# Performance work log

Measured on AMD Instinct MI355X. Metric: run time of the kernel, lower is better.

Reference implementation:

```python
import jax, jax.numpy as jnp
import numpy as np
import math


def setup_inputs() -> dict:
    B, L, D, P, V = 4, 4096, 512, 128, 8
    key = jax.random.key(0)
    ki = iter(jax.random.split(key, 40))
    def rn(shape, s=0.02):
        return jax.random.normal(next(ki), shape, jnp.float32) * s
    z = lambda *s: jnp.zeros(s, jnp.float32)
    return dict(
        x=jax.random.normal(next(ki), (B, L, D), jnp.float32),
        W_omega=rn((D, D)), b_omega=z(D),
        omega_scale=jnp.full((D,), 0.01, jnp.float32),
        W_pi1=rn((D, D)), b_pi1=z(D), W_pi2=rn((D, D)), b_pi2=z(D),
        W_m1v=rn((D, D)), b_m1v=z(D),
        W_m1o=rn((D, D)), b_m1o=z(D),
        W_mag=rn((D, D)), b_mag=z(D),
        mag_scale=jnp.asarray(5.0, jnp.float32),
        W_qoff=rn((D, D)), b_qoff=z(D),
        W_kenc=rn((D, P)), b_kenc=z(P),
        W_venc=rn((D, V)), b_venc=z(V),
        W_sk1=rn((2 * D, D)), b_sk1=z(D),
        W_sk2=rn((D, P)), b_sk2=z(P),
        W_sg=rn((D, 1)), b_sg=z(1),
        W_kvo=rn((V, D)), b_kvo=z(D),
        ln_g=jnp.ones((4 * D,), jnp.float32), ln_b=z(4 * D),
        W_o1=rn((4 * D, 2 * D)), b_o1=z(2 * D),
        W_o2=rn((2 * D, D)), b_o2=z(D),
    )


def _lin(h, W, b):
    return h @ W + b


def _gelu(h):
    return jax.nn.gelu(h, approximate=False)  # torch nn.GELU default (erf)


def _forward(x, W_omega, b_omega, omega_scale, W_pi1, b_pi1, W_pi2, b_pi2,
             W_m1v, b_m1v, W_m1o, b_m1o, W_mag, b_mag, mag_scale,
             W_qoff, b_qoff, W_kenc, b_kenc, W_venc, b_venc,
             W_sk1, b_sk1, W_sk2, b_sk2, W_sg, b_sg, W_kvo, b_kvo,
             ln_g, ln_b, W_o1, b_o1, W_o2, b_o2):
    B, L, D = x.shape
    P = W_kenc.shape[1]
    # --- evolving phases ---
    omega_scaled = _lin(x, W_omega, b_omega) * jnp.abs(omega_scale)
    phi_init = _lin(_gelu(_lin(x, W_pi1, b_pi1)), W_pi2, b_pi2)
    phi = phi_init + jnp.cumsum(omega_scaled, axis=1)
    cos_phi, sin_phi = jnp.cos(phi), jnp.sin(phi)
    # --- memory 1: positional phasor memory ---
    v1 = _lin(x, W_m1v, b_m1v)
    magnitude = jax.nn.sigmoid(_lin(x, W_mag, b_mag)) * jnp.abs(mag_scale)
    wv1 = magnitude * v1
    sqrt_mag = jnp.sqrt(jnp.cumsum(magnitude, axis=1) + 1e-8)
    mem1_cos = jnp.cumsum(wv1 * cos_phi, axis=1) / sqrt_mag
    mem1_sin = jnp.cumsum(wv1 * sin_phi, axis=1) / sqrt_mag
    phi_q = phi + _lin(x, W_qoff, b_qoff)
    pos_ret = (mem1_cos * jnp.cos(phi_q) + mem1_sin * jnp.sin(phi_q)) / math.sqrt(D)
    pos_out = _lin(pos_ret, W_m1o, b_m1o)
    # --- memory 2: key/value phasor binding ---
    query_phase = jnp.tanh(_lin(x, W_kenc, b_kenc)) * math.pi
    values = _lin(x, W_venc, b_venc)                      # [B,L,V]
    store_gate = jax.nn.sigmoid(_lin(x, W_sg, b_sg))      # [B,L,1]
    positions = jnp.arange(1, L + 1, dtype=x.dtype)[None, :, None]
    context_avg = jnp.cumsum(x, axis=1) / positions
    sk_in = jnp.concatenate([x, context_avg], axis=-1)
    storage_phase = jnp.tanh(_lin(_gelu(_lin(sk_in, W_sk1, b_sk1)), W_sk2, b_sk2)) * math.pi
    store_cos, store_sin = jnp.cos(storage_phase), jnp.sin(storage_phase)  # [B,L,P]
    gv = values * store_gate                               # [B,L,V]
    # [B,L,P,V] outer products, cumsum along L
    kv_mem_cos = jnp.cumsum(store_cos[..., None] * gv[:, :, None, :], axis=1)
    kv_mem_sin = jnp.cumsum(store_sin[..., None] * gv[:, :, None, :], axis=1)
    gate_cum = jnp.clip(jnp.cumsum(store_gate, axis=1), 1.0, None)  # [B,L,1]
    inv_norm = (1.0 / jnp.sqrt(gate_cum))[..., None]
    kv_mem_cos = kv_mem_cos * inv_norm
    kv_mem_sin = kv_mem_sin * inv_norm
    q_cos, q_sin = jnp.cos(query_phase), jnp.sin(query_phase)
    kv_retrieved = (jnp.einsum('blp,blpv->blv', q_cos, kv_mem_cos)
                    + jnp.einsum('blp,blpv->blv', q_sin, kv_mem_sin)) / math.sqrt(P)
    kv_out = _lin(kv_retrieved, W_kvo, b_kvo)
    # --- output projection ---
    combined = jnp.concatenate([pos_out, kv_out, x * cos_phi, x * sin_phi], axis=-1)
    mu = combined.mean(axis=-1, keepdims=True)
    var = combined.var(axis=-1, keepdims=True)
    h = (combined - mu) / jnp.sqrt(var + 1e-5) * ln_g + ln_b
    h = _gelu(_lin(h, W_o1, b_o1))  # dropout is identity in eval mode
    return x + _lin(h, W_o2, b_o2)


def reference(x, W_omega, b_omega, omega_scale, W_pi1, b_pi1, W_pi2, b_pi2,
              W_m1v, b_m1v, W_m1o, b_m1o, W_mag, b_mag, mag_scale,
              W_qoff, b_qoff, W_kenc, b_kenc, W_venc, b_venc,
              W_sk1, b_sk1, W_sk2, b_sk2, W_sg, b_sg, W_kvo, b_kvo,
              ln_g, ln_b, W_o1, b_o1, W_o2, b_o2):
    return _forward(x, W_omega, b_omega, omega_scale, W_pi1, b_pi1, W_pi2, b_pi2,
                    W_m1v, b_m1v, W_m1o, b_m1o, W_mag, b_mag, mag_scale,
                    W_qoff, b_qoff, W_kenc, b_kenc, W_venc, b_venc,
                    W_sk1, b_sk1, W_sk2, b_sk2, W_sg, b_sg, W_kvo, b_kvo,
                    ln_g, ln_b, W_o1, b_o1, W_o2, b_o2)
```

## Files before the change

### kernel.cpp

```cpp
#include <hip/hip_runtime.h>
#include <math.h>

#define B_ 4
#define L_ 4096
#define D_ 512
#define P_ 128
#define V_ 8
#define N_ (B_*L_)
#define NC 64
#define CL (L_/NC)
#define LD ((size_t)L_*D_)
#define PI_F 3.14159265358979323846f

typedef unsigned short ushort;
typedef __attribute__((ext_vector_type(8))) short bh8;
typedef __attribute__((ext_vector_type(4))) float f4;
typedef const __attribute__((address_space(1))) unsigned int gu32;
typedef __attribute__((address_space(3))) unsigned int lu32;

__device__ __forceinline__ float geluf(float v){
    return 0.5f*v*(1.0f+erff(v*0.7071067811865475f));
}
__device__ __forceinline__ float tanhf_fast(float x){
    return 1.0f - 2.0f/(__expf(2.0f*x)+1.0f);
}
__device__ __forceinline__ ushort f2b(float f){
    union { float f; unsigned u; } v; v.f = f;
    unsigned r = (v.u + 0x7fffu + ((v.u >> 16) & 1u)) >> 16;
    return (ushort)r;
}
__device__ __forceinline__ float b2f(ushort h){
    union { unsigned u; float f; } v; v.u = ((unsigned)h) << 16;
    return v.f;
}
__device__ __forceinline__ void gload16(const ushort* g, ushort* l){
    __builtin_amdgcn_global_load_lds((gu32*)g, (lu32*)l, 16, 0, 0);
}
__device__ __forceinline__ int xcd_swz(int orig, int nwg){
    int q8 = nwg >> 3, r8 = nwg & 7;
    int xcd = orig & 7, sub = orig >> 3;
    return (xcd < r8 ? xcd*(q8+1) : r8*(q8+1) + (xcd-r8)*q8) + sub;
}

template<int ACT>
__global__ __launch_bounds__(256, 2)
void dgemm_k(const ushort* __restrict__ A, int lda,
             const ushort* __restrict__ Wt, const float* __restrict__ bias,
             ushort* __restrict__ Ob, float* __restrict__ Of,
             int ldc, int K, const float* __restrict__ addbuf)
{
    __shared__ ushort lA[2][128*64];
    __shared__ ushort lB[2][128*64];
    const int tid = threadIdx.x, lane = tid & 63, w = tid >> 6;
    const int wr = w >> 1, wc = w & 1;
    const int nbx = gridDim.x;
    const int wg = xcd_swz(blockIdx.y*nbx + blockIdx.x, nbx*gridDim.y);
    const int row0 = (wg / nbx) * 128, col0 = (wg % nbx) * 128;

    f4 zero4 = {0.f,0.f,0.f,0.f};
    f4 acc[4][4];
    #pragma unroll
    for (int i=0;i<4;i++)
        #pragma unroll
        for (int j=0;j<4;j++) acc[i][j] = zero4;

    auto stage = [&](int buf, int kt){
        #pragma unroll
        for (int is=0; is<4; ++is){
            int id = tid + is*256;
            int r = id >> 3, p = id & 7;
            int srcc = (p ^ (r & 7)) * 8;
            gload16(A + (size_t)(row0 + r)*lda + kt + srcc, &lA[buf][r*64 + p*8]);
        }
        #pragma unroll
        for (int is=0; is<4; ++is){
            int id = tid + is*256;
            int r = id >> 3, p = id & 7;
            int srcc = (p ^ (r & 7)) * 8;
            gload16(Wt + (size_t)(col0 + r)*K + kt + srcc, &lB[buf][r*64 + p*8]);
        }
    };

    const int NT = K >> 6;
    stage(0, 0);
    for (int t2 = 0; t2 < NT; ++t2){
        int cur = t2 & 1;
        if (t2 + 1 < NT){
            stage(cur ^ 1, (t2+1) << 6);
            asm volatile("s_waitcnt vmcnt(8)" ::: "memory");
        } else {
            asm volatile("s_waitcnt vmcnt(0)" ::: "memory");
        }
        __builtin_amdgcn_s_barrier();
        __builtin_amdgcn_sched_barrier(0);
        #pragma unroll
        for (int h=0; h<2; ++h){
            bh8 af[4], bf_[4];
            #pragma unroll
            for (int i=0;i<4;i++){
                int row = wr*64 + i*16 + (lane & 15);
                int pc = (h*4 + (lane >> 4)) ^ (row & 7);
                af[i] = *(const bh8*)&lA[cur][row*64 + pc*8];
            }
            #pragma unroll
            for (int j=0;j<4;j++){
                int row = wc*64 + j*16 + (lane & 15);
                int pc = (h*4 + (lane >> 4)) ^ (row & 7);
                bf_[j] = *(const bh8*)&lB[cur][row*64 + pc*8];
            }
            #pragma unroll
            for (int i=0;i<4;i++)
                #pragma unroll
                for (int j=0;j<4;j++)
                    acc[i][j] = __builtin_amdgcn_mfma_f32_16x16x32_bf16(af[i], bf_[j], acc[i][j], 0, 0, 0);
        }
        __builtin_amdgcn_sched_barrier(0);
        __builtin_amdgcn_s_barrier();
    }

    #pragma unroll
    for (int i=0;i<4;i++){
        int rr = row0 + wr*64 + i*16 + ((lane >> 4) << 2);
        #pragma unroll
        for (int j=0;j<4;j++){
            int cc = col0 + wc*64 + j*16 + (lane & 15);
            float bv = bias[cc];
            #pragma unroll
            for (int q=0;q<4;q++){
                int r = rr + q;
                float t = acc[i][j][q] + bv;
                if (ACT==2){
                    if (addbuf) t += addbuf[(size_t)r*512 + cc];
                    Of[(size_t)r*ldc + cc] = t;
                } else {
                    if (ACT==1) t = geluf(t);
                    Ob[(size_t)r*ldc + cc] = f2b(t);
                }
            }
        }
    }
}

__global__ __launch_bounds__(256, 2)
void fgemm_k(const ushort* __restrict__ A, int lda, const ushort* __restrict__ Wt,
             const float* __restrict__ bs0, const float* __restrict__ bs1,
             const float* __restrict__ bs2, const float* __restrict__ bs3,
             const float* __restrict__ bs4, const float* __restrict__ bs5,
             ushort* __restrict__ o0, ushort* __restrict__ o1p, ushort* __restrict__ o2p,
             ushort* __restrict__ o3p, ushort* __restrict__ o4p,
             ushort* __restrict__ Qc, ushort* __restrict__ Qs,
             const float* __restrict__ omsc, const float* __restrict__ magscp, int K)
{
    __shared__ ushort lA[2][128*32];
    __shared__ ushort lB[2][128*32];
    const int tid = threadIdx.x, lane = tid & 63, w = tid >> 6;
    const int wr = w >> 1, wc = w & 1;
    const int nbx = gridDim.x;
    const int wg = xcd_swz(blockIdx.y*nbx + blockIdx.x, nbx*gridDim.y);
    const int row0 = (wg / nbx) * 128, col0 = (wg % nbx) * 128;

    const int srow = w*32 + (lane >> 2);
    const int scol = (lane & 3) * 8;
    const ushort* gA0 = A  + (size_t)(row0 + srow)      * lda + scol;
    const ushort* gA1 = A  + (size_t)(row0 + srow + 16) * lda + scol;
    const ushort* gB0 = Wt + (size_t)(col0 + srow)      * K   + scol;
    const ushort* gB1 = Wt + (size_t)(col0 + srow + 16) * K   + scol;
    const int d0 = srow*32 + scol, d1 = (srow+16)*32 + scol;

    f4 zero4 = {0.f,0.f,0.f,0.f};
    f4 acc[4][4];
    #pragma unroll
    for (int i=0;i<4;i++)
        #pragma unroll
        for (int j=0;j<4;j++) acc[i][j] = zero4;

    const int fr = lane & 15, fq = (lane >> 4) * 8;
    gload16(gA0, &lA[0][d0]); gload16(gA1, &lA[0][d1]);
    gload16(gB0, &lB[0][d0]); gload16(gB1, &lB[0][d1]);
    __syncthreads();
    int cur = 0;
    for (int kt = 0; kt < K; kt += 32) {
        int nxt = cur ^ 1;
        if (kt + 32 < K) {
            gload16(gA0 + kt + 32, &lA[nxt][d0]); gload16(gA1 + kt + 32, &lA[nxt][d1]);
            gload16(gB0 + kt + 32, &lB[nxt][d0]); gload16(gB1 + kt + 32, &lB[nxt][d1]);
        }
        bh8 af[4], bfr[4];
        #pragma unroll
        for (int i=0;i<4;i++){
            af[i]  = *(const bh8*)&lA[cur][(wr*64 + i*16 + fr)*32 + fq];
            bfr[i] = *(const bh8*)&lB[cur][(wc*64 + i*16 + fr)*32 + fq];
        }
        #pragma unroll
        for (int i=0;i<4;i++)
            #pragma unroll
            for (int j=0;j<4;j++)
                acc[i][j] = __builtin_amdgcn_mfma_f32_16x16x32_bf16(af[i], bfr[j], acc[i][j], 0, 0, 0);
        __syncthreads();
        cur = nxt;
    }

    const int seg = col0 >> 9;
    if (seg == 5) {
        #pragma unroll
        for (int i=0;i<4;i++){
            int rr = row0 + wr*64 + i*16 + ((lane >> 4) << 2);
            #pragma unroll
            for (int j=0;j<4;j++){
                int lcc = (col0 - 2560) + wc*64 + j*16 + (lane & 15);
                float bv = bs5[lcc];
                #pragma unroll
                for (int q=0;q<4;q++){
                    int r = rr + q;
                    float ph = tanhf_fast(acc[i][j][q] + bv)*PI_F;
                    Qc[(size_t)r*128 + lcc] = f2b(__cosf(ph));
                    Qs[(size_t)r*128 + lcc] = f2b(__sinf(ph));
                }
            }
        }
        return;
    }
    const float* bias = seg==0?bs0: seg==1?bs1: seg==2?bs2: seg==3?bs3: bs4;
    ushort* dst = seg==0?o0: seg==1?o1p: seg==2?o2p: seg==3?o3p: o4p;
    float msc = fabsf(*magscp);
    #pragma unroll
    for (int i=0;i<4;i++){
        int rr = row0 + wr*64 + i*16 + ((lane >> 4) << 2);
        #pragma unroll
        for (int j=0;j<4;j++){
            int cc = col0 + wc*64 + j*16 + (lane & 15);
            int lcc = cc & 511;
            float bv = bias[lcc];
            float csc = (seg==0) ? fabsf(omsc[lcc]) : 1.0f;
            #pragma unroll
            for (int q=0;q<4;q++){
                int r = rr + q;
                float t = acc[i][j][q] + bv;
                if (seg==1)      t = msc/(1.0f+__expf(-t));
                else if (seg==3) t = geluf(t);
                else             t *= csc;
                dst[(size_t)r*512 + lcc] = f2b(t);
            }
        }
    }
}

__global__ __launch_bounds__(256, 2)
void mgemm_k(const ushort* __restrict__ Apos, const ushort* __restrict__ Ask,
             const ushort* __restrict__ Wm1o, const ushort* __restrict__ Wsk2,
             const float* __restrict__ bm1o, const float* __restrict__ bsk2,
             ushort* __restrict__ planes, ushort* __restrict__ Kc, ushort* __restrict__ Ks)
{
    __shared__ ushort lA[2][128*32];
    __shared__ ushort lB[2][128*32];
    const int tid = threadIdx.x, lane = tid & 63, w = tid >> 6;
    const int wr = w >> 1, wc = w & 1;
    const int nbx = gridDim.x;
    const int wg = xcd_swz(blockIdx.y*nbx + blockIdx.x, nbx*gridDim.y);
    const int row0 = (wg / nbx) * 128, col0 = (wg % nbx) * 128;
    const int seg = col0 >> 9;
    const ushort* A  = seg ? Ask  : Apos;
    const ushort* Wt = seg ? Wsk2 : Wm1o;
    const int wcol0 = seg ? (col0 - 512) : col0;
    const int K = 512;

    const int srow = w*32 + (lane >> 2);
    const int scol = (lane & 3) * 8;
    const ushort* gA0 = A  + (size_t)(row0 + srow)       * 512 + scol;
    const ushort* gA1 = A  + (size_t)(row0 + srow + 16)  * 512 + scol;
    const ushort* gB0 = Wt + (size_t)(wcol0 + srow)      * 512 + scol;
    const ushort* gB1 = Wt + (size_t)(wcol0 + srow + 16) * 512 + scol;
    const int d0 = srow*32 + scol, d1 = (srow+16)*32 + scol;

    f4 zero4 = {0.f,0.f,0.f,0.f};
    f4 acc[4][4];
    #pragma unroll
    for (int i=0;i<4;i++)
        #pragma unroll
        for (int j=0;j<4;j++) acc[i][j] = zero4;

    const int fr = lane & 15, fq = (lane >> 4) * 8;
    gload16(gA0, &lA[0][d0]); gload16(gA1, &lA[0][d1]);
    gload16(gB0, &lB[0][d0]); gload16(gB1, &lB[0][d1]);
    __syncthreads();
    int cur = 0;
    for (int kt = 0; kt < K; kt += 32) {
        int nxt = cur ^ 1;
        if (kt + 32 < K) {
            gload16(gA0 + kt + 32, &lA[nxt][d0]); gload16(gA1 + kt + 32, &lA[nxt][d1]);
            gload16(gB0 + kt + 32, &lB[nxt][d0]); gload16(gB1 + kt + 32, &lB[nxt][d1]);
        }
        bh8 af[4], bfr[4];
        #pragma unroll
        for (int i=0;i<4;i++){
            af[i]  = *(const bh8*)&lA[cur][(wr*64 + i*16 + fr)*32 + fq];
            bfr[i] = *(const bh8*)&lB[cur][(wc*64 + i*16 + fr)*32 + fq];
        }
        #pragma unroll
        for (int i=0;i<4;i++)
            #pragma unroll
            for (int j=0;j<4;j++)
                acc[i][j] = __builtin_amdgcn_mfma_f32_16x16x32_bf16(af[i], bfr[j], acc[i][j], 0, 0, 0);
        __syncthreads();
        cur = nxt;
    }

    #pragma unroll
    for (int i=0;i<4;i++){
        int rr = row0 + wr*64 + i*16 + ((lane >> 4) << 2);
        #pragma unroll
        for (int j=0;j<4;j++){
            int cc = col0 + wc*64 + j*16 + (lane & 15);
            #pragma unroll
            for (int q=0;q<4;q++){
                int r = rr + q;
                if (seg == 0){
                    planes[(size_t)r*2048 + cc] = f2b(acc[i][j][q] + bm1o[cc]);
                } else {
                    int lcc = cc - 512;
                    float ph = tanhf_fast(acc[i][j][q] + bsk2[lcc])*PI_F;
                    Kc[(size_t)r*128 + lcc] = f2b(__cosf(ph));
                    Ks[(size_t)r*128 + lcc] = f2b(__sinf(ph));
                }
            }
        }
    }
}

struct WtArgs {
    const float* src[12];
    ushort* dst[12];
    int K[12], M[12], t0[13];
};
__global__ __launch_bounds__(256)
void wtall_k(WtArgs a)
{
    __shared__ float tile[32][33];
    int bb = blockIdx.x;
    int j = 0;
    while (bb >= a.t0[j+1]) ++j;
    int tt = bb - a.t0[j];
    int K = a.K[j], M = a.M[j];
    int mt = M >> 5;
    int kb = (tt / mt) * 32, mb = (tt % mt) * 32;
    const float* W = a.src[j]; ushort* Wt = a.dst[j];
    int tx = threadIdx.x & 31, ty = threadIdx.x >> 5;
    #pragma unroll
    for (int i = ty; i < 32; i += 8)
        tile[i][tx] = W[(size_t)(kb+i)*M + mb+tx];
    __syncthreads();
    #pragma unroll
    for (int i = ty; i < 32; i += 8)
        Wt[(size_t)(mb+i)*K + kb+tx] = f2b(tile[tx][i]);
}

__global__ __launch_bounds__(256)
void fconv_k(const float* __restrict__ in, ushort* __restrict__ xctx)
{
    size_t i = ((size_t)blockIdx.x*256 + threadIdx.x) * 4;
    size_t row = i >> 9; int d = (int)(i & 511);
    float4 v = *(const float4*)(in + i);
    ushort* o = xctx + row*1024 + d;
    o[0]=f2b(v.x); o[1]=f2b(v.y); o[2]=f2b(v.z); o[3]=f2b(v.w);
}

__global__ __launch_bounds__(256)
void s1a_k(const ushort* __restrict__ omega, const float* __restrict__ xg,
           float* __restrict__ csA, float* __restrict__ csX)
{
    int bid = blockIdx.x;
    int b = bid >> 7; int rem = bid & 127;
    int dg = rem & 1, c = rem >> 1;
    int d = dg*256 + threadIdx.x;
    size_t base = ((size_t)b*L_ + (size_t)c*CL)*D_ + d;
    float sA=0.f, sX=0.f;
    for (int l=0;l<CL;l++){
        sA += b2f(omega[base + (size_t)l*D_]);
        sX += xg[base + (size_t)l*D_];
    }
    size_t ci = ((size_t)b*NC + c)*D_ + d;
    csA[ci]=sA; csX[ci]=sX;
}

__global__ __launch_bounds__(256)
void aux1_k(float* __restrict__ csA, float* __restrict__ csX,
            const float* __restrict__ sgate, float* __restrict__ rinv, int nb2)
{
    __shared__ float wsum[4];
    __shared__ float carry;
    int bb = blockIdx.x, t = threadIdx.x;
    if (bb < nb2){
        int tt = bb*256 + t;
        int b = tt >> 9, d = tt & 511;
        float* bufs[2] = {csA, csX};
        #pragma unroll
        for (int i=0;i<2;i++){
            float* p = bufs[i] + ((size_t)b*NC)*D_ + d;
            float run=0.f;
            for (int c=0;c<NC;c++){
                float v = p[(size_t)c*D_];
                p[(size_t)c*D_] = run;
                run += v;
            }
        }
        return;
    }
    int b = bb - nb2;
    int lane = t & 63, wave = t >> 6;
    if (t == 0) carry = 0.f;
    __syncthreads();
    for (int s = 0; s < L_/256; s++){
        float v = sgate[(size_t)b*L_ + s*256 + t];
        float sc = v;
        #pragma unroll
        for (int off=1; off<64; off<<=1){
            float u = __shfl_up(sc, off, 64);
            if (lane >= off) sc += u;
        }
        if (lane == 63) wsum[wave] = sc;
        __syncthreads();
        float woff = carry;
        for (int w2 = 0; w2 < wave; w2++) woff += wsum[w2];
        float inc = sc + woff;
        rinv[(size_t)b*L_ + s*256 + t] = rsqrtf(fmaxf(inc, 1.0f));
        __syncthreads();
        if (t == 255) carry = inc;
        __syncthreads();
    }
}

__global__ void prefix_k(float* a, float* b2v, float* c3, int nbuf)
{
    int t = blockIdx.x*blockDim.x + threadIdx.x;
    int b = t >> 9, d = t & 511;
    float* bufs[3] = {a,b2v,c3};
    for (int i=0;i<nbuf;i++){
        float* p = bufs[i] + ((size_t)b*NC)*D_ + d;
        float run=0.f;
        for (int c=0;c<NC;c++){
            float v = p[(size_t)c*D_];
            p[(size_t)c*D_] = run;
            run += v;
        }
    }
}

__global__ __launch_bounds__(256)
void s1c_k(const ushort* __restrict__ omega, const float* __restrict__ xg,
           const ushort* __restrict__ phi_init,
           const ushort* __restrict__ magn, const ushort* __restrict__ v1,
           const float* __restrict__ csA, const float* __restrict__ csX,
           ushort* __restrict__ cphi, ushort* __restrict__ sphi, ushort* __restrict__ xctx,
           float* __restrict__ csM, float* __restrict__ csC, float* __restrict__ csS)
{
    int bid = blockIdx.x;
    int b = bid >> 7; int rem = bid & 127;
    int dg = rem & 1, c = rem >> 1;
    int d = dg*256 + threadIdx.x;
    size_t ci = ((size_t)b*NC + c)*D_ + d;
    float phiacc = csA[ci], xacc = csX[ci];
    float sM=0.f,sC=0.f,sS=0.f;
    size_t xrow = (size_t)b*L_ + (size_t)c*CL;
    size_t base = xrow*D_ + d;
    for (int l=0;l<CL;l++){
        size_t idx = base + (size_t)l*D_;
        phiacc += b2f(omega[idx]);
        float ph = b2f(phi_init[idx]) + phiacc;
        float spv = __sinf(ph), cpv = __cosf(ph);
        cphi[idx] = f2b(cpv); sphi[idx] = f2b(spv);
        xacc += xg[idx];
        xctx[(xrow + l)*1024 + 512 + d] = f2b(__fdividef(xacc, (float)(c*CL + l + 1)));
        float m = b2f(magn[idx]); sM += m;
        float wv = m * b2f(v1[idx]);
        sC = fmaf(wv, cpv, sC); sS = fmaf(wv, spv, sS);
    }
    csM[ci]=sM; csC[ci]=sC; csS[ci]=sS;
}

__global__ __launch_bounds__(256)
void s1e_k(const ushort* __restrict__ magn, const ushort* __restrict__ v1,
           const ushort* qoff, const ushort* __restrict__ cphi, const ushort* __restrict__ sphi,
           const float* __restrict__ csM, const float* __restrict__ csC,
           const float* __restrict__ csS, ushort* pos_ret)
{
    int bid = blockIdx.x;
    int b = bid >> 7; int rem = bid & 127;
    int dg = rem & 1, c = rem >> 1;
    int d = dg*256 + threadIdx.x;
    size_t ci = ((size_t)b*NC + c)*D_ + d;
    float mA=csM[ci], cA=csC[ci], sA=csS[ci];
    size_t base = ((size_t)b*L_ + (size_t)c*CL)*D_ + d;
    for (int l=0;l<CL;l++){
        size_t idx = base + (size_t)l*D_;
        float m = b2f(magn[idx]); mA += m;
        float wv = m * b2f(v1[idx]);
        float cp = b2f(cphi[idx]), sp = b2f(sphi[idx]);
        cA = fmaf(wv, cp, cA); sA = fmaf(wv, sp, sA);
        float rs = rsqrtf(mA + 1e-8f);
        float qo = b2f(qoff[idx]);
        float sq = __sinf(qo), cq = __cosf(qo);
        float cosq = cp*cq - sp*sq;
        float sinq = sp*cq + cp*sq;
        pos_ret[idx] = f2b((cA*cosq + sA*sinq) * rs * 0.04419417382415922f);
    }
}

__global__ __launch_bounds__(256)
void vencsg_k(const float* __restrict__ xg, const float* __restrict__ Wv,
              const float* __restrict__ bv, const float* __restrict__ Wg,
              const float* __restrict__ bg,
              ushort* __restrict__ gvb, float* __restrict__ sgate)
{
    int gw = (int)((blockIdx.x*(size_t)blockDim.x + threadIdx.x) >> 6);
    int lane = threadIdx.x & 63;
    const float* xr = xg + (size_t)gw*D_;
    float pv[8] = {0,0,0,0,0,0,0,0}; float pg = 0.f;
    #pragma unroll
    for (int j=0;j<8;j++){
        int k = lane + 64*j;
        float xv = xr[k];
        #pragma unroll
        for (int v=0;v<8;v++) pv[v] = fmaf(xv, Wv[k*8+v], pv[v]);
        pg = fmaf(xv, Wg[k], pg);
    }
    #pragma unroll
    for (int off=32; off>0; off>>=1){
        #pragma unroll
        for (int v=0;v<8;v++) pv[v] += __shfl_down(pv[v], off, 64);
        pg += __shfl_down(pg, off, 64);
    }
    if (lane==0){
        float sg = 1.0f/(1.0f+__expf(-(pg + bg[0])));
        #pragma unroll
        for (int v=0;v<8;v++) gvb[(size_t)gw*8+v] = f2b((pv[v] + bv[v]) * sg);
        sgate[gw] = sg;
    }
}

__global__ __launch_bounds__(256)
void kvsum_k(const ushort* __restrict__ Kc, const ushort* __restrict__ Ks,
             const ushort* __restrict__ gvb, float* __restrict__ csKV)
{
    int bid = blockIdx.x;
    int b = bid >> 6, c = bid & 63;
    int t = threadIdx.x; int p = t & 127; int v0 = (t>>7)*4;
    size_t row0 = (size_t)b*L_ + (size_t)c*64;
    float ac[4]={0,0,0,0}, as[4]={0,0,0,0};
    for (int l=0;l<64;l++){
        size_t r = row0 + l;
        float kc = b2f(Kc[r*(size_t)P_ + p]);
        float ks = b2f(Ks[r*(size_t)P_ + p]);
        #pragma unroll
        for (int j=0;j<4;j++){
            float gv = b2f(gvb[r*(size_t)V_ + v0 + j]);
            ac[j] = fmaf(kc, gv, ac[j]);
            as[j] = fmaf(ks, gv, as[j]);
        }
    }
    float* base = csKV + ((size_t)b*64 + c)*2048;
    #pragma unroll
    for (int j=0;j<4;j++){
        base[p*V_ + v0 + j] = ac[j];
        base[1024 + p*V_ + v0 + j] = as[j];
    }
}

__global__ void kvpfx_k(float* __restrict__ csKV)
{
    int t = blockIdx.x*blockDim.x + threadIdx.x;
    int b = t >> 11, si = t & 2047;
    float* ptr = csKV + ((size_t)b*64)*2048 + si;
    float run=0.f;
    for (int c=0;c<64;c++){
        float v = ptr[(size_t)c*2048];
        ptr[(size_t)c*2048] = run;
        run += v;
    }
}

__global__ __launch_bounds__(256)
void kv2_k(const ushort* __restrict__ Qc, const ushort* __restrict__ Qs,
           const ushort* __restrict__ Kc, const ushort* __restrict__ Ks,
           const ushort* __restrict__ gvb, const float* __restrict__ rinv,
           const float* __restrict__ csKV, float* __restrict__ kvret)
{
    __shared__ ushort sS[64][66];
    __shared__ float sM[2048];
    __shared__ float sgv[64][8];
    int tile = blockIdx.x, b = blockIdx.y;
    int t = threadIdx.x, lane = t & 63, w = t >> 6;
    int wr = w >> 1, wc = w & 1;
    size_t row0 = (size_t)b*L_ + (size_t)tile*64;
    const float* kvb = csKV + ((size_t)b*64 + tile)*2048;
    #pragma unroll
    for (int k=0;k<8;k++) sM[t + k*256] = kvb[t + k*256];
    #pragma unroll
    for (int k=0;k<2;k++){
        int idx = t + k*256; int l = idx >> 3, v = idx & 7;
        sgv[l][v] = b2f(gvb[(row0 + l)*(size_t)V_ + v]);
    }
    f4 zero4 = {0.f,0.f,0.f,0.f};
    f4 acc[2][2];
    #pragma unroll
    for (int i=0;i<2;i++)
        #pragma unroll
        for (int j=0;j<2;j++) acc[i][j] = zero4;
    #pragma unroll
    for (int ks=0; ks<8; ks++){
        const ushort* Ab = (ks<4) ? Qc : Qs;
        const ushort* Bb = (ks<4) ? Kc : Ks;
        int kb = (ks&3)*32 + (lane>>4)*8;
        bh8 af[2], bfr[2];
        #pragma unroll
        for (int i=0;i<2;i++)
            af[i] = *(const bh8*)(Ab + (row0 + wr*32 + i*16 + (lane&15))*(size_t)P_ + kb);
        #pragma unroll
        for (int j=0;j<2;j++)
            bfr[j] = *(const bh8*)(Bb + (row0 + wc*32 + j*16 + (lane&15))*(size_t)P_ + kb);
        #pragma unroll
        for (int i=0;i<2;i++)
            #pragma unroll
            for (int j=0;j<2;j++)
                acc[i][j] = __builtin_amdgcn_mfma_f32_16x16x32_bf16(af[i], bfr[j], acc[i][j], 0, 0, 0);
    }
    #pragma unroll
    for (int i=0;i<2;i++){
        #pragma unroll
        for (int j=0;j<2;j++){
            int cc = wc*32 + j*16 + (lane & 15);
            #pragma unroll
            for (int q=0;q<4;q++){
                int lr = wr*32 + i*16 + ((lane>>4)<<2) + q;
                sS[lr][cc] = f2b((cc <= lr) ? acc[i][j][q] : 0.f);
            }
        }
    }
    __syncthreads();
    int l = t & 63, vh = t >> 6; int v0 = vh*2;
    const ushort* qcr = Qc + (row0 + l)*(size_t)P_;
    const ushort* qsr = Qs + (row0 + l)*(size_t)P_;
    float a0=0.f, a1=0.f;
    #pragma unroll
    for (int pc=0; pc<16; pc++){
        bh8 qc8 = *(const bh8*)(qcr + pc*8);
        bh8 qs8 = *(const bh8*)(qsr + pc*8);
        #pragma unroll
        for (int e=0;e<8;e++){
            int p = pc*8+e;
            float qc = b2f((ushort)qc8[e]), qs = b2f((ushort)qs8[e]);
            a0 += qc*sM[p*8+v0]   + qs*sM[1024+p*8+v0];
            a1 += qc*sM[p*8+v0+1] + qs*sM[1024+p*8+v0+1];
        }
    }
    for (int c=0;c<64;c++){
        float sv = b2f(sS[l][c]);
        a0 = fmaf(sv, sgv[c][v0],   a0);
        a1 = fmaf(sv, sgv[c][v0+1], a1);
    }
    float rn = rinv[row0 + l] * 0.08838834764831845f;
    kvret[(row0+l)*(size_t)V_ + v0]   = a0*rn;
    kvret[(row0+l)*(size_t)V_ + v0+1] = a1*rn;
}

__global__ __launch_bounds__(256)
void cmb_k(const float* __restrict__ xg, const ushort* __restrict__ cphi,
           const ushort* __restrict__ sphi,
           const float* __restrict__ kvret, const float* __restrict__ Wkvo,
           const float* __restrict__ bkvo,
           const float* __restrict__ ln_g, const float* __restrict__ ln_b,
           ushort* pl)
{
    __shared__ float red[8];
    __shared__ float kvv[8];
    int n = blockIdx.x; int t = threadIdx.x;
    int wave = t>>6, lane = t&63;
    if (t < 8) kvv[t] = kvret[(size_t)n*8 + t];
    __syncthreads();
    float v_[8]; float sum=0.f, sumsq=0.f;
    #pragma unroll
    for (int i=0;i<8;i++){
        int cidx = t + i*256;
        int seg = cidx >> 9, cc = cidx & 511;
        float v;
        if (seg == 0) v = b2f(pl[(size_t)n*2048 + cidx]);
        else if (seg == 1) {
            v = bkvo[cc];
            #pragma unroll
            for (int vv=0; vv<8; vv++) v = fmaf(kvv[vv], Wkvo[vv*512 + cc], v);
        } else {
            size_t id = (size_t)n*D_ + cc;
            v = xg[id] * b2f((seg==2) ? cphi[id] : sphi[id]);
        }
        v_[i]=v; sum += v; sumsq = fmaf(v,v,sumsq);
    }
    #pragma unroll
    for (int off=32; off>0; off>>=1){
        sum += __shfl_xor(sum, off, 64);
        sumsq += __shfl_xor(sumsq, off, 64);
    }
    if (lane==0){ red[wave]=sum; red[wave+4]=sumsq; }
    __syncthreads();
    float s = red[0]+red[1]+red[2]+red[3];
    float q = red[4]+red[5]+red[6]+red[7];
    float mu = s * (1.0f/2048.0f);
    float var = q * (1.0f/2048.0f) - mu*mu;
    float rstd = rsqrtf(var + 1e-5f);
    #pragma unroll
    for (int i=0;i<8;i++){
        int cidx = t + i*256;
        float h = (v_[i]-mu)*rstd*ln_g[cidx] + ln_b[cidx];
        pl[(size_t)n*2048 + cidx] = f2b(h);
    }
}

__global__ void copyx_k(const float* __restrict__ x, float* __restrict__ out, size_t n)
{
    size_t i = (size_t)blockIdx.x*256 + threadIdx.x;
    if (i < n) out[i] = x[i];
}

struct WS {
    ushort *wt_fused,*wt_pi2,*wt_sk1,*wt_sk2,*wt_m1o,*wt_o1,*wt_o2;
    ushort *xctx, *pool;
    ushort *Qc,*Qs,*Kc,*Ks,*gvb,*cphi,*sphi;
    float *sgate,*rinv,*kvret;
    float *csA,*csX,*csM,*csC,*csS,*csKV;
};

static size_t ws_layout(WS& w, char* base, int NB)
{
    size_t off = 0;
    auto al = [&](size_t bytes)->char* {
        char* p = base + off; off = (off + bytes + 255) & ~(size_t)255; return p;
    };
    size_t R = (size_t)NB * L_;
    w.wt_fused=(ushort*)al((size_t)2688*512*2);
    w.wt_pi2 =(ushort*)al(512*512*2);
    w.wt_sk1 =(ushort*)al((size_t)512*1024*2); w.wt_sk2=(ushort*)al(128*512*2);
    w.wt_m1o =(ushort*)al(512*512*2);
    w.wt_o1  =(ushort*)al((size_t)1024*2048*2); w.wt_o2=(ushort*)al((size_t)512*1024*2);
    w.xctx=(ushort*)al(R*1024*2);
    w.pool=(ushort*)al(R*512*2*6);
    w.Qc=(ushort*)al(R*128*2); w.Qs=(ushort*)al(R*128*2);
    w.Kc=(ushort*)al(R*128*2); w.Ks=(ushort*)al(R*128*2);
    w.gvb=(ushort*)al(R*8*2);
    w.cphi=(ushort*)al(R*512*2); w.sphi=(ushort*)al(R*512*2);
    w.sgate=(float*)al(R*4); w.rinv=(float*)al(R*4); w.kvret=(float*)al(R*8*4);
    w.csA=(float*)al((size_t)NB*NC*512*4); w.csX=(float*)al((size_t)NB*NC*512*4);
    w.csM=(float*)al((size_t)NB*NC*512*4); w.csC=(float*)al((size_t)NB*NC*512*4);
    w.csS=(float*)al((size_t)NB*NC*512*4);
    w.csKV=(float*)al((size_t)NB*64*2048*4);
    return off;
}

extern "C" void kernel_launch(void* const* d_in, const int* in_sizes, int n_in,
                              void* d_out, int out_size, void* d_ws, size_t ws_size,
                              hipStream_t stream)
{
    const float* x        =(const float*)d_in[0];
    const float* W_omega  =(const float*)d_in[1];  const float* b_omega=(const float*)d_in[2];
    const float* omega_sc =(const float*)d_in[3];
    const float* W_pi1    =(const float*)d_in[4];  const float* b_pi1 =(const float*)d_in[5];
    const float* W_pi2    =(const float*)d_in[6];  const float* b_pi2 =(const float*)d_in[7];
    const float* W_m1v    =(const float*)d_in[8];  const float* b_m1v =(const float*)d_in[9];
    const float* W_m1o    =(const float*)d_in[10]; const float* b_m1o =(const float*)d_in[11];
    const float* W_mag    =(const float*)d_in[12]; const float* b_mag =(const float*)d_in[13];
    const float* mag_sc   =(const float*)d_in[14];
    const float* W_qoff   =(const float*)d_in[15]; const float* b_qoff=(const float*)d_in[16];
    const float* W_kenc   =(const float*)d_in[17]; const float* b_kenc=(const float*)d_in[18];
    const float* W_venc   =(const float*)d_in[19]; const float* b_venc=(const float*)d_in[20];
    const float* W_sk1    =(const float*)d_in[21]; const float* b_sk1 =(const float*)d_in[22];
    const float* W_sk2    =(const float*)d_in[23]; const float* b_sk2 =(const float*)d_in[24];
    const float* W_sg     =(const float*)d_in[25]; const float* b_sg  =(const float*)d_in[26];
    const float* W_kvo    =(const float*)d_in[27]; const float* b_kvo =(const float*)d_in[28];
    const float* ln_g     =(const float*)d_in[29]; const float* ln_b  =(const float*)d_in[30];
    const float* W_o1     =(const float*)d_in[31]; const float* b_o1  =(const float*)d_in[32];
    const float* W_o2     =(const float*)d_in[33]; const float* b_o2  =(const float*)d_in[34];
    float* out = (float*)d_out;

    char* wsb = (char*)d_ws;
    WS w;
    int NB = 4;
    if (ws_layout(w, wsb, 4) > ws_size) {
        NB = 2;
        if (ws_layout(w, wsb, 2) > ws_size) {
            NB = 1;
            if (ws_layout(w, wsb, 1) > ws_size) {
                copyx_k<<<dim3((unsigned)(((size_t)N_*D_ + 255)/256)), dim3(256), 0, stream>>>(x, out, (size_t)N_*D_);
                return;
            }
        }
    }

    dim3 blk(256);
    WtArgs wa;
    const float* srcs[12] = {W_omega, W_mag, W_m1v, W_pi1, W_qoff, W_kenc,
                             W_pi2, W_sk1, W_sk2, W_m1o, W_o1, W_o2};
    ushort* dsts[12] = {w.wt_fused + (size_t)0*512*512, w.wt_fused + (size_t)1*512*512,
                        w.wt_fused + (size_t)2*512*512, w.wt_fused + (size_t)3*512*512,
                        w.wt_fused + (size_t)4*512*512, w.wt_fused + (size_t)5*512*512,
                        w.wt_pi2, w.wt_sk1, w.wt_sk2, w.wt_m1o, w.wt_o1, w.wt_o2};
    int Ks_[12] = {512,512,512,512,512,512, 512,1024,512,512,2048,1024};
    int Ms_[12] = {512,512,512,512,512,128, 512, 512,128,512,1024, 512};
    int cum = 0;
    for (int j = 0; j < 12; ++j){
        wa.src[j]=srcs[j]; wa.dst[j]=dsts[j]; wa.K[j]=Ks_[j]; wa.M[j]=Ms_[j];
        wa.t0[j]=cum; cum += (Ks_[j]/32)*(Ms_[j]/32);
    }
    wa.t0[12]=cum;
    wtall_k<<<dim3(cum), blk, 0, stream>>>(wa);

    const int R = NB * L_;
    const size_t SL = (size_t)R * 512;
    ushort* bA = w.pool;        ushort* bB = w.pool + SL;
    ushort* bC = w.pool + 2*SL; ushort* bD = w.pool + 3*SL;
    ushort* bE = w.pool + 4*SL; ushort* bF = w.pool + 5*SL;
    ushort* planes = w.pool;
    ushort* h1 = w.pool + 4*SL;

    #define DGEMM(ACT,A,lda,Wt_,bias_,Ob_,Of_,ldc,K_,M_,add_) \
        dgemm_k<ACT><<<dim3((M_)/128, R/128), blk, 0, stream>>>(A,lda,Wt_,bias_,Ob_,Of_,ldc,K_,add_)

    for (int g = 0; g < B_/NB; ++g) {
        const float* xg = x + (size_t)g*NB*LD;
        float* outg = out + (size_t)g*NB*LD;

        fconv_k<<<dim3((unsigned)((size_t)R*512/1024)), blk, 0, stream>>>(xg, w.xctx);

        fgemm_k<<<dim3(2688/128, R/128), blk, 0, stream>>>(
            w.xctx,1024, w.wt_fused, b_omega,b_mag,b_m1v,b_pi1,b_qoff,b_kenc,
            bA,bB,bC,bD,bF, w.Qc,w.Qs, omega_sc, mag_sc, 512);
        DGEMM(0, bD,512, w.wt_pi2, b_pi2, bE,(float*)0, 512, 512,512, (const float*)0);
        vencsg_k<<<dim3((unsigned)((size_t)R*64/256)), blk, 0, stream>>>(xg, W_venc,b_venc, W_sg,b_sg, w.gvb, w.sgate);
        s1a_k<<<dim3(NB*NC*2), blk, 0, stream>>>(bA, xg, w.csA, w.csX);
        aux1_k<<<dim3(NB*2 + NB), blk, 0, stream>>>(w.csA, w.csX, w.sgate, w.rinv, NB*2);
        s1c_k<<<dim3(NB*NC*2), blk, 0, stream>>>(bA, xg, bE, bB, bC, w.csA, w.csX,
                                                 w.cphi, w.sphi, w.xctx, w.csM, w.csC, w.csS);
        prefix_k<<<dim3(NB*2), blk, 0, stream>>>(w.csM, w.csC, w.csS, 3);
        s1e_k<<<dim3(NB*NC*2), blk, 0, stream>>>(bB, bC, bF, w.cphi, w.sphi,
                                                 w.csM, w.csC, w.csS, bF);

        DGEMM(1, w.xctx,1024, w.wt_sk1, b_sk1, bD,(float*)0, 512, 1024,512, (const float*)0);
        mgemm_k<<<dim3(640/128, R/128), blk, 0, stream>>>(
            bF, bD, w.wt_m1o, w.wt_sk2, b_m1o, b_sk2, planes, w.Kc, w.Ks);

        kvsum_k<<<dim3(NB*64), blk, 0, stream>>>(w.Kc, w.Ks, w.gvb, w.csKV);
        kvpfx_k<<<dim3(NB*8), blk, 0, stream>>>(w.csKV);
        kv2_k<<<dim3(64, NB), blk, 0, stream>>>(w.Qc, w.Qs, w.Kc, w.Ks, w.gvb, w.rinv, w.csKV, w.kvret);

        cmb_k<<<dim3(R), blk, 0, stream>>>(xg, w.cphi, w.sphi, w.kvret, W_kvo, b_kvo,
                                           ln_g, ln_b, planes);
        DGEMM(1, planes,2048, w.wt_o1, b_o1, h1,(float*)0, 1024, 2048,1024, (const float*)0);
        DGEMM(2, h1,1024, w.wt_o2, b_o2, (ushort*)0,outg, 512, 1024,512, xg);
    }
    #undef DGEMM
}
```

Before: 477.6 us.

## Swizzle GEMM LDS tiles and read bf16 x copy instead of fp32 input

Applies an XOR swizzle to the shared-memory layout in fgemm_k and mgemm_k so that the MFMA fragment reads spread across LDS banks instead of conflicting. Separately, several elementwise kernels (s1a, s1c, vencsg, cmb) now read the bf16 copy of x held in xctx rather than the fp32 input, halving that traffic. The sk1 GEMM output buffer changes from bD to bE, presumably to avoid aliasing with later use. Reading x in bf16 lowers the precision of the x-dependent terms such as x*cos_phi and the running mean of x.

```diff
diff --git a/kernel.cpp b/kernel.cpp
--- a/kernel.cpp
+++ b/kernel.cpp
@@ -160,12 +160,13 @@
     const int row0 = (wg / nbx) * 128, col0 = (wg % nbx) * 128;
 
     const int srow = w*32 + (lane >> 2);
-    const int scol = (lane & 3) * 8;
-    const ushort* gA0 = A  + (size_t)(row0 + srow)      * lda + scol;
-    const ushort* gA1 = A  + (size_t)(row0 + srow + 16) * lda + scol;
-    const ushort* gB0 = Wt + (size_t)(col0 + srow)      * K   + scol;
-    const ushort* gB1 = Wt + (size_t)(col0 + srow + 16) * K   + scol;
-    const int d0 = srow*32 + scol, d1 = (srow+16)*32 + scol;
+    const int sch  = lane & 3;
+    const int scolA = (sch ^ (srow & 3)) * 8;
+    const ushort* gA0 = A  + (size_t)(row0 + srow)      * lda + scolA;
+    const ushort* gA1 = A  + (size_t)(row0 + srow + 16) * lda + scolA;
+    const ushort* gB0 = Wt + (size_t)(col0 + srow)      * K   + scolA;
+    const ushort* gB1 = Wt + (size_t)(col0 + srow + 16) * K   + scolA;
+    const int d0 = srow*32 + sch*8, d1 = (srow+16)*32 + sch*8;
 
     f4 zero4 = {0.f,0.f,0.f,0.f};
     f4 acc[4][4];
@@ -174,7 +175,8 @@
         #pragma unroll
         for (int j=0;j<4;j++) acc[i][j] = zero4;
 
-    const int fr = lane & 15, fq = (lane >> 4) * 8;
+    const int fr = lane & 15;
+    const int pcr = (((lane >> 4) ^ (fr & 3))) * 8;
     gload16(gA0, &lA[0][d0]); gload16(gA1, &lA[0][d1]);
     gload16(gB0, &lB[0][d0]); gload16(gB1, &lB[0][d1]);
     __syncthreads();
@@ -188,8 +190,8 @@
         bh8 af[4], bfr[4];
         #pragma unroll
         for (int i=0;i<4;i++){
-            af[i]  = *(const bh8*)&lA[cur][(wr*64 + i*16 + fr)*32 + fq];
-            bfr[i] = *(const bh8*)&lB[cur][(wc*64 + i*16 + fr)*32 + fq];
+            af[i]  = *(const bh8*)&lA[cur][(wr*64 + i*16 + fr)*32 + pcr];
+            bfr[i] = *(const bh8*)&lB[cur][(wc*64 + i*16 + fr)*32 + pcr];
         }
         #pragma unroll
         for (int i=0;i<4;i++)
@@ -265,12 +267,13 @@
     const int K = 512;
 
     const int srow = w*32 + (lane >> 2);
-    const int scol = (lane & 3) * 8;
-    const ushort* gA0 = A  + (size_t)(row0 + srow)       * 512 + scol;
-    const ushort* gA1 = A  + (size_t)(row0 + srow + 16)  * 512 + scol;
-    const ushort* gB0 = Wt + (size_t)(wcol0 + srow)      * 512 + scol;
-    const ushort* gB1 = Wt + (size_t)(wcol0 + srow + 16) * 512 + scol;
-    const int d0 = srow*32 + scol, d1 = (srow+16)*32 + scol;
+    const int sch  = lane & 3;
+    const int scolA = (sch ^ (srow & 3)) * 8;
+    const ushort* gA0 = A  + (size_t)(row0 + srow)       * 512 + scolA;
+    const ushort* gA1 = A  + (size_t)(row0 + srow + 16)  * 512 + scolA;
+    const ushort* gB0 = Wt + (size_t)(wcol0 + srow)      * 512 + scolA;
+    const ushort* gB1 = Wt + (size_t)(wcol0 + srow + 16) * 512 + scolA;
+    const int d0 = srow*32 + sch*8, d1 = (srow+16)*32 + sch*8;
 
     f4 zero4 = {0.f,0.f,0.f,0.f};
     f4 acc[4][4];
@@ -279,7 +282,8 @@
         #pragma unroll
         for (int j=0;j<4;j++) acc[i][j] = zero4;
 
-    const int fr = lane & 15, fq = (lane >> 4) * 8;
+    const int fr = lane & 15;
+    const int pcr = (((lane >> 4) ^ (fr & 3))) * 8;
     gload16(gA0, &lA[0][d0]); gload16(gA1, &lA[0][d1]);
     gload16(gB0, &lB[0][d0]); gload16(gB1, &lB[0][d1]);
     __syncthreads();
@@ -293,8 +297,8 @@
         bh8 af[4], bfr[4];
         #pragma unroll
         for (int i=0;i<4;i++){
-            af[i]  = *(const bh8*)&lA[cur][(wr*64 + i*16 + fr)*32 + fq];
-            bfr[i] = *(const bh8*)&lB[cur][(wc*64 + i*16 + fr)*32 + fq];
+            af[i]  = *(const bh8*)&lA[cur][(wr*64 + i*16 + fr)*32 + pcr];
+            bfr[i] = *(const bh8*)&lB[cur][(wc*64 + i*16 + fr)*32 + pcr];
         }
         #pragma unroll
         for (int i=0;i<4;i++)
@@ -365,18 +369,19 @@
 }
 
 __global__ __launch_bounds__(256)
-void s1a_k(const ushort* __restrict__ omega, const float* __restrict__ xg,
+void s1a_k(const ushort* __restrict__ omega, const ushort* __restrict__ xctx,
            float* __restrict__ csA, float* __restrict__ csX)
 {
     int bid = blockIdx.x;
     int b = bid >> 7; int rem = bid & 127;
     int dg = rem & 1, c = rem >> 1;
     int d = dg*256 + threadIdx.x;
-    size_t base = ((size_t)b*L_ + (size_t)c*CL)*D_ + d;
+    size_t row0 = (size_t)b*L_ + (size_t)c*CL;
+    size_t base = row0*D_ + d;
     float sA=0.f, sX=0.f;
     for (int l=0;l<CL;l++){
         sA += b2f(omega[base + (size_t)l*D_]);
-        sX += xg[base + (size_t)l*D_];
+        sX += b2f(xctx[(row0 + l)*1024 + d]);
     }
     size_t ci = ((size_t)b*NC + c)*D_ + d;
     csA[ci]=sA; csX[ci]=sX;
@@ -446,8 +451,7 @@
 }
 
 __global__ __launch_bounds__(256)
-void s1c_k(const ushort* __restrict__ omega, const float* __restrict__ xg,
-           const ushort* __restrict__ phi_init,
+void s1c_k(const ushort* __restrict__ omega, const ushort* __restrict__ phi_init,
            const ushort* __restrict__ magn, const ushort* __restrict__ v1,
            const float* __restrict__ csA, const float* __restrict__ csX,
            ushort* __restrict__ cphi, ushort* __restrict__ sphi, ushort* __restrict__ xctx,
@@ -468,7 +472,7 @@
         float ph = b2f(phi_init[idx]) + phiacc;
         float spv = __sinf(ph), cpv = __cosf(ph);
         cphi[idx] = f2b(cpv); sphi[idx] = f2b(spv);
-        xacc += xg[idx];
+        xacc += b2f(xctx[(xrow + l)*1024 + d]);
         xctx[(xrow + l)*1024 + 512 + d] = f2b(__fdividef(xacc, (float)(c*CL + l + 1)));
         float m = b2f(magn[idx]); sM += m;
         float wv = m * b2f(v1[idx]);
@@ -506,19 +510,19 @@
 }
 
 __global__ __launch_bounds__(256)
-void vencsg_k(const float* __restrict__ xg, const float* __restrict__ Wv,
+void vencsg_k(const ushort* __restrict__ xctx, const float* __restrict__ Wv,
               const float* __restrict__ bv, const float* __restrict__ Wg,
               const float* __restrict__ bg,
               ushort* __restrict__ gvb, float* __restrict__ sgate)
 {
     int gw = (int)((blockIdx.x*(size_t)blockDim.x + threadIdx.x) >> 6);
     int lane = threadIdx.x & 63;
-    const float* xr = xg + (size_t)gw*D_;
+    const ushort* xr = xctx + (size_t)gw*1024;
     float pv[8] = {0,0,0,0,0,0,0,0}; float pg = 0.f;
     #pragma unroll
     for (int j=0;j<8;j++){
         int k = lane + 64*j;
-        float xv = xr[k];
+        float xv = b2f(xr[k]);
         #pragma unroll
         for (int v=0;v<8;v++) pv[v] = fmaf(xv, Wv[k*8+v], pv[v]);
         pg = fmaf(xv, Wg[k], pg);
@@ -663,7 +667,7 @@
 }
 
 __global__ __launch_bounds__(256)
-void cmb_k(const float* __restrict__ xg, const ushort* __restrict__ cphi,
+void cmb_k(const ushort* __restrict__ xctx, const ushort* __restrict__ cphi,
            const ushort* __restrict__ sphi,
            const float* __restrict__ kvret, const float* __restrict__ Wkvo,
            const float* __restrict__ bkvo,
@@ -689,7 +693,7 @@
             for (int vv=0; vv<8; vv++) v = fmaf(kvv[vv], Wkvo[vv*512 + cc], v);
         } else {
             size_t id = (size_t)n*D_ + cc;
-            v = xg[id] * b2f((seg==2) ? cphi[id] : sphi[id]);
+            v = b2f(xctx[(size_t)n*1024 + cc]) * b2f((seg==2) ? cphi[id] : sphi[id]);
         }
         v_[i]=v; sum += v; sumsq = fmaf(v,v,sumsq);
     }
@@ -831,24 +835,24 @@
             w.xctx,1024, w.wt_fused, b_omega,b_mag,b_m1v,b_pi1,b_qoff,b_kenc,
             bA,bB,bC,bD,bF, w.Qc,w.Qs, omega_sc, mag_sc, 512);
         DGEMM(0, bD,512, w.wt_pi2, b_pi2, bE,(float*)0, 512, 512,512, (const float*)0);
-        vencsg_k<<<dim3((unsigned)((size_t)R*64/256)), blk, 0, stream>>>(xg, W_venc,b_venc, W_sg,b_sg, w.gvb, w.sgate);
-        s1a_k<<<dim3(NB*NC*2), blk, 0, stream>>>(bA, xg, w.csA, w.csX);
+        vencsg_k<<<dim3((unsigned)((size_t)R*64/256)), blk, 0, stream>>>(w.xctx, W_venc,b_venc, W_sg,b_sg, w.gvb, w.sgate);
+        s1a_k<<<dim3(NB*NC*2), blk, 0, stream>>>(bA, w.xctx, w.csA, w.csX);
         aux1_k<<<dim3(NB*2 + NB), blk, 0, stream>>>(w.csA, w.csX, w.sgate, w.rinv, NB*2);
-        s1c_k<<<dim3(NB*NC*2), blk, 0, stream>>>(bA, xg, bE, bB, bC, w.csA, w.csX,
+        s1c_k<<<dim3(NB*NC*2), blk, 0, stream>>>(bA, bE, bB, bC, w.csA, w.csX,
                                                  w.cphi, w.sphi, w.xctx, w.csM, w.csC, w.csS);
         prefix_k<<<dim3(NB*2), blk, 0, stream>>>(w.csM, w.csC, w.csS, 3);
         s1e_k<<<dim3(NB*NC*2), blk, 0, stream>>>(bB, bC, bF, w.cphi, w.sphi,
                                                  w.csM, w.csC, w.csS, bF);
 
-        DGEMM(1, w.xctx,1024, w.wt_sk1, b_sk1, bD,(float*)0, 512, 1024,512, (const float*)0);
+        DGEMM(1, w.xctx,1024, w.wt_sk1, b_sk1, bE,(float*)0, 512, 1024,512, (const float*)0);
         mgemm_k<<<dim3(640/128, R/128), blk, 0, stream>>>(
-            bF, bD, w.wt_m1o, w.wt_sk2, b_m1o, b_sk2, planes, w.Kc, w.Ks);
+            bF, bE, w.wt_m1o, w.wt_sk2, b_m1o, b_sk2, planes, w.Kc, w.Ks);
 
         kvsum_k<<<dim3(NB*64), blk, 0, stream>>>(w.Kc, w.Ks, w.gvb, w.csKV);
         kvpfx_k<<<dim3(NB*8), blk, 0, stream>>>(w.csKV);
         kv2_k<<<dim3(64, NB), blk, 0, stream>>>(w.Qc, w.Qs, w.Kc, w.Ks, w.gvb, w.rinv, w.csKV, w.kvret);
 
-        cmb_k<<<dim3(R), blk, 0, stream>>>(xg, w.cphi, w.sphi, w.kvret, W_kvo, b_kvo,
+        cmb_k<<<dim3(R), blk, 0, stream>>>(w.xctx, w.cphi, w.sphi, w.kvret, W_kvo, b_kvo,
                                            ln_g, ln_b, planes);
         DGEMM(1, planes,2048, w.wt_o1, b_o1, h1,(float*)0, 1024, 2048,1024, (const float*)0);
         DGEMM(2, h1,1024, w.wt_o2, b_o2, (ushort*)0,outg, 512, 1024,512, xg);
```

Measured after the change: 476.1 us. About the same (-0.3%).
